# Optimization experiments

Measured on AMD Instinct MI355X. Metric: run time of the kernel, lower is better.

Reference implementation:

```python
import jax, jax.numpy as jnp
import numpy as np

VOCAB, EMB, HID = 50000, 128, 128
BATCH, SEQ = 256, 2048


def setup_inputs() -> dict:
    key = jax.random.key(0)
    k1, k2, k3, k4, k5 = jax.random.split(key, 5)
    x = jax.random.randint(k1, (BATCH, SEQ), 0, VOCAB, dtype=jnp.int32)
    emb_table = jax.random.normal(k2, (VOCAB, EMB), dtype=jnp.float32) * 0.05
    # Keras GRU (reset_after=True): kernel (EMB, 3H), recurrent_kernel (H, 3H),
    # bias (2, 3H) = [input_bias, recurrent_bias]; gate order z, r, h.
    W = jax.random.normal(k3, (EMB, 3 * HID), dtype=jnp.float32) * (1.0 / np.sqrt(EMB))
    U = jax.random.normal(k4, (HID, 3 * HID), dtype=jnp.float32) * (1.0 / np.sqrt(HID))
    b = jax.random.normal(k5, (2, 3 * HID), dtype=jnp.float32) * 0.01
    return {"x": x, "emb_table": emb_table, "W": W, "U": U, "b": b}


def _gru_scan(emb, W, U, b):
    # emb: (B, T, E). Precompute all input projections in one big GEMM.
    B, T, _ = emb.shape
    H = U.shape[0]
    xw = jnp.einsum("bte,eh->bth", emb, W) + b[0]  # (B, T, 3H)

    def step(h, xw_t):
        rh = h @ U + b[1]                      # (B, 3H) recurrent projection
        xz, xr, xh = jnp.split(xw_t, 3, axis=-1)
        uz, ur, uh = jnp.split(rh, 3, axis=-1)
        z = jax.nn.sigmoid(xz + uz)
        r = jax.nn.sigmoid(xr + ur)
        hh = jnp.tanh(xh + r * uh)             # reset_after=True candidate
        h_new = z * h + (1.0 - z) * hh
        return h_new, h_new

    h0 = jnp.zeros((B, H), dtype=emb.dtype)
    state, outs = jax.lax.scan(step, h0, jnp.swapaxes(xw, 0, 1))  # outs: (T, B, H)
    return jnp.swapaxes(outs, 0, 1), state


def reference(x, emb_table, W, U, b):
    emb = emb_table[x]                         # (B, T, E) embedding gather
    output, state = _gru_scan(emb, W, U, b)
    # V1 and V2 compute identical math -> diff is exactly zero.
    max_diff = jnp.zeros((), dtype=output.dtype)
    outputs_close = jnp.array(True)
    return output, state, outputs_close, max_diff
```

## Files before the change

### kernel.cpp

```cpp
#include <hip/hip_runtime.h>

#define B_ 256
#define T_ 2048
#define E_ 128
#define H_ 128
#define NC 384

typedef short bf16x8 __attribute__((ext_vector_type(8)));
typedef float f32x4  __attribute__((ext_vector_type(4)));

#define MF(A_, B2_, C_) __builtin_amdgcn_mfma_f32_16x16x32_bf16((A_), (B2_), (C_), 0, 0, 0)

static __device__ __forceinline__ unsigned short f2bf(float f) {
    unsigned u = __builtin_bit_cast(unsigned, f);
    return (unsigned short)((u + 0x7FFFu + ((u >> 16) & 1u)) >> 16);
}
static __device__ __forceinline__ float bf2f(unsigned short h) {
    unsigned u = (unsigned)h << 16;
    return __builtin_bit_cast(float, u);
}
static __device__ __forceinline__ float xhalf(float v, int addr) {
    return __builtin_bit_cast(float,
        __builtin_amdgcn_ds_bpermute(addr, __builtin_bit_cast(int, v)));
}
static __device__ __forceinline__ float fexp2(float x) {
    float r;
    asm("v_exp_f32 %0, %1" : "=v"(r) : "v"(x));
    return r;
}
static __device__ __forceinline__ float frcp(float x) {
    float r;
    asm("v_rcp_f32 %0, %1" : "=v"(r) : "v"(x));
    return r;
}

__global__ __launch_bounds__(512) __attribute__((amdgpu_waves_per_eu(2, 2)))
void gru_xw_mfma(
    const int*   __restrict__ x,
    const float* __restrict__ emb,
    const float* __restrict__ W,
    const float* __restrict__ bias,
    unsigned short* __restrict__ xw,
    int t0, int nsteps)
{
    const int p    = blockIdx.x;
    const int tid  = threadIdx.x;
    const int w    = tid >> 6;
    const int lane = tid & 63;
    const int rowA = lane & 15;
    const int q    = lane >> 4;
    const int mh   = w >> 2;
    const int nq   = w & 3;

    __shared__ unsigned short A_lds[2][64 * 128];

    bf16x8 Wf[6][4];
    float bf6[6]; int offn[6];
    #pragma unroll
    for (int nt = 0; nt < 6; ++nt) {
        const int col = nq * 96 + nt * 16 + rowA;
        const int g = col >> 7, cc = col & 127;
        bf6[nt]  = bias[col] + (g < 2 ? bias[NC + col] : 0.f);
        offn[nt] = (g == 2) ? (256 + cc) : ((cc << 1) + g);
        #pragma unroll
        for (int kt = 0; kt < 4; ++kt)
            #pragma unroll
            for (int e = 0; e < 8; ++e) {
                const int k = (kt << 5) + ((e >> 2) << 4) + (q << 2) + (e & 3);
                Wf[nt][kt][e] = (short)f2bf(W[(size_t)k * NC + col]);
            }
    }

    const int niter = nsteps >> 6;
    const int r_st  = tid >> 3;
    const int j_st  = tid & 7;

    #pragma unroll 1
    for (int it = 0; it < niter; ++it) {
        const int rowbase = p * nsteps + (it << 6);

        {
            const int row_local = rowbase + r_st;
            const int tloc = row_local >> 8, bb = row_local & 255;
            const int token = x[bb * T_ + t0 + tloc];
            const float* erow = emb + (size_t)token * E_;
            unsigned* dst = (unsigned*)A_lds[it & 1];
            const int mt = r_st >> 4, rA = r_st & 15;
            #pragma unroll
            for (int s = 0; s < 8; ++s) {
                const int p2 = j_st + (s << 3);
                const float2 ev = *(const float2*)(erow + (p2 << 1));
                const int kt = p2 >> 4, hi = (p2 >> 3) & 1;
                const int qq = (p2 >> 1) & 3, l0 = p2 & 1;
                const int dw = (((mt << 2) + kt) * 64 + rA + (qq << 4)) * 4
                             + (hi << 1) + l0;
                dst[dw] = (unsigned)f2bf(ev.x) | ((unsigned)f2bf(ev.y) << 16);
            }
        }
        asm volatile("s_waitcnt lgkmcnt(0)" ::: "memory");
        __builtin_amdgcn_s_barrier();
        asm volatile("" ::: "memory");

        const unsigned short* src = A_lds[it & 1];
        bf16x8 Af[2][4];
        #pragma unroll
        for (int ml = 0; ml < 2; ++ml)
            #pragma unroll
            for (int kt = 0; kt < 4; ++kt)
                Af[ml][kt] = *(const bf16x8*)(src +
                    ((((2 * mh + ml) << 2) + kt) * 64 + lane) * 8);

        f32x4 acc[2][6];
        #pragma unroll
        for (int ml = 0; ml < 2; ++ml)
            #pragma unroll
            for (int nt = 0; nt < 6; ++nt) {
                f32x4 a = {0.f, 0.f, 0.f, 0.f};
                a = MF(Af[ml][0], Wf[nt][0], a);
                a = MF(Af[ml][1], Wf[nt][1], a);
                a = MF(Af[ml][2], Wf[nt][2], a);
                a = MF(Af[ml][3], Wf[nt][3], a);
                acc[ml][nt] = a;
            }

        #pragma unroll
        for (int ml = 0; ml < 2; ++ml)
            #pragma unroll
            for (int reg = 0; reg < 4; ++reg) {
                const int m = (mh << 5) + (ml << 4) + (q << 2) + reg;
                const int row_local = rowbase + m;
                const int tloc = row_local >> 8, bb = row_local & 255;
                unsigned short* orow = xw + ((size_t)tloc * B_ + bb) * 384;
                #pragma unroll
                for (int nt = 0; nt < 6; ++nt)
                    orow[offn[nt]] = f2bf(acc[ml][nt][reg] + bf6[nt]);
            }
    }
}

__global__ __launch_bounds__(256) __attribute__((amdgpu_waves_per_eu(1, 1)))
void gru_rec_kernel(
    const unsigned short* __restrict__ xw,
    const float* __restrict__ U,
    const float* __restrict__ bias,
    float*       __restrict__ out,
    float*       __restrict__ hstate,
    int t0, int nsteps, int last)
{
    const int b   = blockIdx.x;
    const int tid = threadIdx.x;
    const int w   = tid >> 6;
    const int l   = tid & 63;
    const int col = (w << 5) + (l & 31);
    const int kh  = l >> 5;

    __shared__ __align__(16) unsigned h_pk[2][64];
    __shared__ __align__(16) unsigned short xwt[2][8][384];

    unsigned Upk[3][32];
    #pragma unroll
    for (int g = 0; g < 3; ++g) {
        #pragma unroll
        for (int j = 0; j < 32; ++j) {
            const int k = (kh << 6) + (j << 1);
            const unsigned short lo = f2bf(U[(size_t)k * NC + (g << 7) + col]);
            const unsigned short hi = f2bf(U[(size_t)(k + 1) * NC + (g << 7) + col]);
            Upk[g][j] = (unsigned)lo | ((unsigned)hi << 16);
        }
    }

    const float b1h = bias[NC + 256 + col];
    float hreg = (t0 == 0) ? 0.f : hstate[(b << 7) + col];
    if (l < 32) ((unsigned short*)h_pk[0])[col] = f2bf(hreg);

    const int srow = tid >> 5;
    const int sj   = tid & 31;
    const unsigned short* ld0 = xw + ((size_t)srow * B_ + b) * 384 + sj * 12;
    uint2 sA = *(const uint2*)(ld0);
    uint2 sB = *(const uint2*)(ld0 + 4);
    uint2 sC = *(const uint2*)(ld0 + 8);
    {
        unsigned short* dst = &xwt[0][srow][sj * 12];
        *(uint2*)dst = sA; *(uint2*)(dst + 4) = sB; *(uint2*)(dst + 8) = sC;
    }
    const int ntiles = nsteps >> 3;
    if (1 < ntiles) {
        const unsigned short* p1 = xw + ((size_t)(8 + srow) * B_ + b) * 384 + sj * 12;
        sA = *(const uint2*)(p1); sB = *(const uint2*)(p1 + 4); sC = *(const uint2*)(p1 + 8);
    }
    __syncthreads();

    float* outb = out + ((size_t)b * T_ + t0) * H_;
    const int xaddr = (l ^ 32) << 2;
    const float NL2E = -1.4426950408889634f;
    const float P2L2E = 2.8853900817779268f;

#define RSTEP(GS, XROW)                                                        \
    do {                                                                       \
        const uint4* hsrc = (const uint4*)(h_pk[(GS) & 1] + (kh << 5));        \
        const uint4 q0 = hsrc[0], q1 = hsrc[1], q2 = hsrc[2], q3 = hsrc[3];    \
        const uint4 q4 = hsrc[4], q5 = hsrc[5], q6 = hsrc[6], q7 = hsrc[7];    \
        const unsigned hd[32] = {q0.x, q0.y, q0.z, q0.w, q1.x, q1.y, q1.z, q1.w,\
                                 q2.x, q2.y, q2.z, q2.w, q3.x, q3.y, q3.z, q3.w,\
                                 q4.x, q4.y, q4.z, q4.w, q5.x, q5.y, q5.z, q5.w,\
                                 q6.x, q6.y, q6.z, q6.w, q7.x, q7.y, q7.z, q7.w};\
        const int zr = *(const int*)((XROW) + (col << 1));            \
        const unsigned short xh16 = (XROW)[256 + col];                \
        float a0 = 0.f, a1 = 0.f, a2 = 0.f;                                    \
        float c0 = 0.f, c1 = 0.f, c2 = 0.f;                                    \
        _Pragma("unroll")                                                      \
        for (int j = 0; j < 32; j += 2) {                                      \
            asm("v_dot2_f32_bf16 %0, %1, %2, %0"                               \
                : "+v"(a0) : "v"(Upk[0][j]), "v"(hd[j]));                      \
            asm("v_dot2_f32_bf16 %0, %1, %2, %0"                               \
                : "+v"(a1) : "v"(Upk[1][j]), "v"(hd[j]));                      \
            asm("v_dot2_f32_bf16 %0, %1, %2, %0"                               \
                : "+v"(a2) : "v"(Upk[2][j]), "v"(hd[j]));                      \
            asm("v_dot2_f32_bf16 %0, %1, %2, %0"                               \
                : "+v"(c0) : "v"(Upk[0][j + 1]), "v"(hd[j + 1]));              \
            asm("v_dot2_f32_bf16 %0, %1, %2, %0"                               \
                : "+v"(c1) : "v"(Upk[1][j + 1]), "v"(hd[j + 1]));              \
            asm("v_dot2_f32_bf16 %0, %1, %2, %0"                               \
                : "+v"(c2) : "v"(Upk[2][j + 1]), "v"(hd[j + 1]));              \
        }                                                                      \
        a0 += c0; a1 += c1; a2 += c2;                                          \
        a0 += xhalf(a0, xaddr);             \
        a1 += xhalf(a1, xaddr);                                                \
        a2 += xhalf(a2, xaddr);                                                \
        const float xz = bf2f((unsigned short)(zr & 0xFFFF));                  \
        const float xr = bf2f((unsigned short)((unsigned)zr >> 16));           \
        const float xh = bf2f(xh16);                                           \
        const float z = frcp(1.f + fexp2(NL2E * (xz + a0)));                   \
        const float r = frcp(1.f + fexp2(NL2E * (xr + a1)));                   \
        float aa = xh + r * (a2 + b1h);                                        \
        aa = fminf(30.f, fmaxf(-30.f, aa));                                    \
        const float e2 = fexp2(P2L2E * aa);                                    \
        const float th = 1.f - 2.f * frcp(e2 + 1.f);                           \
        hreg = z * hreg + (1.f - z) * th;                                      \
        if (l < 32) {                                                          \
            ((unsigned short*)h_pk[((GS) + 1) & 1])[col] = f2bf(hreg);         \
            outb[(size_t)(GS) * H_ + col] = hreg;         \
        }                                                                      \
        asm volatile("s_waitcnt lgkmcnt(0)" ::: "memory");                     \
        __builtin_amdgcn_s_barrier();                                          \
        asm volatile("" ::: "memory");                                         \
    } while (0)

    #pragma unroll 1
    for (int tile = 0; tile < ntiles; ++tile) {
        const int cur = tile & 1;
        if (tile + 1 < ntiles) {
            unsigned short* dst = &xwt[cur ^ 1][srow][sj * 12];
            *(uint2*)dst = sA; *(uint2*)(dst + 4) = sB; *(uint2*)(dst + 8) = sC;
            if (tile + 2 < ntiles) {
                const unsigned short* pn =
                    xw + ((size_t)((tile + 2) * 8 + srow) * B_ + b) * 384 + sj * 12;
                sA = *(const uint2*)(pn);
                sB = *(const uint2*)(pn + 4);
                sC = *(const uint2*)(pn + 8);
            }
        }
        const int gbase = tile << 3;
        #pragma unroll
        for (int s = 0; s < 8; ++s) {
            RSTEP(gbase + s, &xwt[cur][s][0]);
        }
    }
#undef RSTEP

    if (l < 32) {
        hstate[(b << 7) + col] = hreg;
        if (last) out[(size_t)B_ * T_ * H_ + (b << 7) + col] = hreg;
    }
    if (last && b == 0 && tid == 0) {
        const size_t base = (size_t)B_ * T_ * H_ + (size_t)B_ * H_;
        out[base]     = 1.0f;
        out[base + 1] = 0.0f;
    }
}

extern "C" void kernel_launch(void* const* d_in, const int* in_sizes, int n_in,
                              void* d_out, int out_size, void* d_ws, size_t ws_size,
                              hipStream_t stream)
{
    const int*   x   = (const int*)  d_in[0];
    const float* emb = (const float*)d_in[1];
    const float* W   = (const float*)d_in[2];
    const float* U   = (const float*)d_in[3];
    const float* bi  = (const float*)d_in[4];
    float* out = (float*)d_out;

    unsigned short* xwbuf = (unsigned short*)d_ws;
    const size_t perstep = (size_t)B_ * 384 * sizeof(unsigned short);
    const size_t hbytes  = (size_t)B_ * H_ * sizeof(float);

    size_t avail = (ws_size > hbytes) ? (ws_size - hbytes) : 0;
    long long chunk_ll = (long long)(avail / perstep);
    int chunk = (chunk_ll > T_) ? T_ : (int)chunk_ll;
    chunk &= ~63;
    if (chunk < 64) chunk = 64;

    float* hstate = (float*)((char*)d_ws + (size_t)chunk * perstep);

    for (int t0 = 0; t0 < T_; t0 += chunk) {
        const int n = (T_ - t0 < chunk) ? (T_ - t0) : chunk;
        const int last = (t0 + n >= T_) ? 1 : 0;
        hipLaunchKernelGGL(gru_xw_mfma, dim3(B_), dim3(512), 0, stream,
                           x, emb, W, bi, xwbuf, t0, n);
        hipLaunchKernelGGL(gru_rec_kernel, dim3(B_), dim3(256), 0, stream,
                           xwbuf, U, bi, out, hstate, t0, n, last);
    }
}
```

Before: 1.184 ms.

## Assign one thread per hidden column in recurrent GRU kernel, drop cross-lane reduce

The recurrent kernel now uses 128 threads per block, with each thread computing the full 128-long dot products for its column instead of splitting K across two half-waves. This removes the ds_bpermute reduction and halves the number of waves synchronising at each per-step barrier. Packing bf16 h pairs into LDS uses a DPP lane swap, and xw staging uses wider 16-byte loads. The trade-off is twice as many serial dot2 instructions and LDS reads per thread on the per-step critical path, plus higher register use for U.

```diff
diff --git a/kernel.cpp b/kernel.cpp
--- a/kernel.cpp
+++ b/kernel.cpp
@@ -19,9 +19,8 @@
     unsigned u = (unsigned)h << 16;
     return __builtin_bit_cast(float, u);
 }
-static __device__ __forceinline__ float xhalf(float v, int addr) {
-    return __builtin_bit_cast(float,
-        __builtin_amdgcn_ds_bpermute(addr, __builtin_bit_cast(int, v)));
+static __device__ __forceinline__ unsigned dpp_x1_u(unsigned v) {
+    return (unsigned)__builtin_amdgcn_mov_dpp((int)v, 0xB1, 0xF, 0xF, true);
 }
 static __device__ __forceinline__ float fexp2(float x) {
     float r;
@@ -138,7 +137,7 @@
     }
 }
 
-__global__ __launch_bounds__(256) __attribute__((amdgpu_waves_per_eu(1, 1)))
+__global__ __launch_bounds__(128) __attribute__((amdgpu_waves_per_eu(1, 1)))
 void gru_rec_kernel(
     const unsigned short* __restrict__ xw,
     const float* __restrict__ U,
@@ -149,20 +148,17 @@
 {
     const int b   = blockIdx.x;
     const int tid = threadIdx.x;
-    const int w   = tid >> 6;
-    const int l   = tid & 63;
-    const int col = (w << 5) + (l & 31);
-    const int kh  = l >> 5;
+    const int col = tid;
 
     __shared__ __align__(16) unsigned h_pk[2][64];
     __shared__ __align__(16) unsigned short xwt[2][8][384];
 
-    unsigned Upk[3][32];
+    unsigned Upk[3][64];
     #pragma unroll
     for (int g = 0; g < 3; ++g) {
         #pragma unroll
-        for (int j = 0; j < 32; ++j) {
-            const int k = (kh << 6) + (j << 1);
+        for (int j = 0; j < 64; ++j) {
+            const int k = j << 1;
             const unsigned short lo = f2bf(U[(size_t)k * NC + (g << 7) + col]);
             const unsigned short hi = f2bf(U[(size_t)(k + 1) * NC + (g << 7) + col]);
             Upk[g][j] = (unsigned)lo | ((unsigned)hi << 16);
@@ -171,76 +167,83 @@
 
     const float b1h = bias[NC + 256 + col];
     float hreg = (t0 == 0) ? 0.f : hstate[(b << 7) + col];
-    if (l < 32) ((unsigned short*)h_pk[0])[col] = f2bf(hreg);
-
-    const int srow = tid >> 5;
-    const int sj   = tid & 31;
-    const unsigned short* ld0 = xw + ((size_t)srow * B_ + b) * 384 + sj * 12;
-    uint2 sA = *(const uint2*)(ld0);
-    uint2 sB = *(const uint2*)(ld0 + 4);
-    uint2 sC = *(const uint2*)(ld0 + 8);
     {
-        unsigned short* dst = &xwt[0][srow][sj * 12];
-        *(uint2*)dst = sA; *(uint2*)(dst + 4) = sB; *(uint2*)(dst + 8) = sC;
+        const unsigned me = (unsigned)f2bf(hreg);
+        const unsigned pk = me | (dpp_x1_u(me) << 16);
+        if (!(col & 1)) h_pk[0][col >> 1] = pk;
+    }
+
+    const int srow = tid >> 4;
+    const int sj   = tid & 15;
+    const unsigned short* ld0 = xw + ((size_t)srow * B_ + b) * 384 + sj * 24;
+    uint4 sA = *(const uint4*)(ld0);
+    uint4 sB = *(const uint4*)(ld0 + 8);
+    uint4 sC = *(const uint4*)(ld0 + 16);
+    {
+        unsigned short* dst = &xwt[0][srow][sj * 24];
+        *(uint4*)dst = sA; *(uint4*)(dst + 8) = sB; *(uint4*)(dst + 16) = sC;
     }
     const int ntiles = nsteps >> 3;
     if (1 < ntiles) {
-        const unsigned short* p1 = xw + ((size_t)(8 + srow) * B_ + b) * 384 + sj * 12;
-        sA = *(const uint2*)(p1); sB = *(const uint2*)(p1 + 4); sC = *(const uint2*)(p1 + 8);
+        const unsigned short* p1 =
+            xw + ((size_t)(8 + srow) * B_ + b) * 384 + sj * 24;
+        sA = *(const uint4*)(p1); sB = *(const uint4*)(p1 + 8); sC = *(const uint4*)(p1 + 16);
     }
     __syncthreads();
 
     float* outb = out + ((size_t)b * T_ + t0) * H_;
-    const int xaddr = (l ^ 32) << 2;
     const float NL2E = -1.4426950408889634f;
     const float P2L2E = 2.8853900817779268f;
 
 #define RSTEP(GS, XROW)                                                        \
     do {                                                                       \
-        const uint4* hsrc = (const uint4*)(h_pk[(GS) & 1] + (kh << 5));        \
-        const uint4 q0 = hsrc[0], q1 = hsrc[1], q2 = hsrc[2], q3 = hsrc[3];    \
-        const uint4 q4 = hsrc[4], q5 = hsrc[5], q6 = hsrc[6], q7 = hsrc[7];    \
-        const unsigned hd[32] = {q0.x, q0.y, q0.z, q0.w, q1.x, q1.y, q1.z, q1.w,\
-                                 q2.x, q2.y, q2.z, q2.w, q3.x, q3.y, q3.z, q3.w,\
-                                 q4.x, q4.y, q4.z, q4.w, q5.x, q5.y, q5.z, q5.w,\
-                                 q6.x, q6.y, q6.z, q6.w, q7.x, q7.y, q7.z, q7.w};\
-        const int zr = *(const int*)((XROW) + (col << 1));            \
-        const unsigned short xh16 = (XROW)[256 + col];                \
-        float a0 = 0.f, a1 = 0.f, a2 = 0.f;                                    \
-        float c0 = 0.f, c1 = 0.f, c2 = 0.f;                                    \
+        const uint4* hsrc = (const uint4*)h_pk[(GS) & 1];                      \
+        float az0 = 0.f, ar0 = 0.f, ah0 = 0.f;                                 \
+        float az1 = 0.f, ar1 = 0.f, ah1 = 0.f;                                 \
         _Pragma("unroll")                                                      \
-        for (int j = 0; j < 32; j += 2) {                                      \
-            asm("v_dot2_f32_bf16 %0, %1, %2, %0"                               \
-                : "+v"(a0) : "v"(Upk[0][j]), "v"(hd[j]));                      \
-            asm("v_dot2_f32_bf16 %0, %1, %2, %0"                               \
-                : "+v"(a1) : "v"(Upk[1][j]), "v"(hd[j]));                      \
-            asm("v_dot2_f32_bf16 %0, %1, %2, %0"                               \
-                : "+v"(a2) : "v"(Upk[2][j]), "v"(hd[j]));                      \
-            asm("v_dot2_f32_bf16 %0, %1, %2, %0"                               \
-                : "+v"(c0) : "v"(Upk[0][j + 1]), "v"(hd[j + 1]));              \
-            asm("v_dot2_f32_bf16 %0, %1, %2, %0"                               \
-                : "+v"(c1) : "v"(Upk[1][j + 1]), "v"(hd[j + 1]));              \
-            asm("v_dot2_f32_bf16 %0, %1, %2, %0"                               \
-                : "+v"(c2) : "v"(Upk[2][j + 1]), "v"(hd[j + 1]));              \
+        for (int c4 = 0; c4 < 4; ++c4) {            \
+            const uint4 hq0 = hsrc[(c4 << 2) + 0];                             \
+            const uint4 hq1 = hsrc[(c4 << 2) + 1];                             \
+            const uint4 hq2 = hsrc[(c4 << 2) + 2];                             \
+            const uint4 hq3 = hsrc[(c4 << 2) + 3];                             \
+            const unsigned hv[16] = {hq0.x, hq0.y, hq0.z, hq0.w,               \
+                                     hq1.x, hq1.y, hq1.z, hq1.w,               \
+                                     hq2.x, hq2.y, hq2.z, hq2.w,               \
+                                     hq3.x, hq3.y, hq3.z, hq3.w};              \
+            _Pragma("unroll")                                                  \
+            for (int i = 0; i < 16; i += 2) {                                  \
+                const int j = (c4 << 4) + i;                                   \
+                asm("v_dot2_f32_bf16 %0, %1, %2, %0"                           \
+                    : "+v"(az0) : "v"(Upk[0][j]), "v"(hv[i]));                 \
+                asm("v_dot2_f32_bf16 %0, %1, %2, %0"                           \
+                    : "+v"(ar0) : "v"(Upk[1][j]), "v"(hv[i]));                 \
+                asm("v_dot2_f32_bf16 %0, %1, %2, %0"                           \
+                    : "+v"(ah0) : "v"(Upk[2][j]), "v"(hv[i]));                 \
+                asm("v_dot2_f32_bf16 %0, %1, %2, %0"                           \
+                    : "+v"(az1) : "v"(Upk[0][j + 1]), "v"(hv[i + 1]));         \
+                asm("v_dot2_f32_bf16 %0, %1, %2, %0"                           \
+                    : "+v"(ar1) : "v"(Upk[1][j + 1]), "v"(hv[i + 1]));         \
+                asm("v_dot2_f32_bf16 %0, %1, %2, %0"                           \
+                    : "+v"(ah1) : "v"(Upk[2][j + 1]), "v"(hv[i + 1]));         \
+            }                                                                  \
         }                                                                      \
-        a0 += c0; a1 += c1; a2 += c2;                                          \
-        a0 += xhalf(a0, xaddr);             \
-        a1 += xhalf(a1, xaddr);                                                \
-        a2 += xhalf(a2, xaddr);                                                \
+        const float s0 = az0 + az1, s1 = ar0 + ar1, s2 = ah0 + ah1;            \
+        const int zr = ((const int*)(XROW))[col];                              \
+        const unsigned short xh16 = (XROW)[256 + col];                         \
         const float xz = bf2f((unsigned short)(zr & 0xFFFF));                  \
         const float xr = bf2f((unsigned short)((unsigned)zr >> 16));           \
         const float xh = bf2f(xh16);                                           \
-        const float z = frcp(1.f + fexp2(NL2E * (xz + a0)));                   \
-        const float r = frcp(1.f + fexp2(NL2E * (xr + a1)));                   \
-        float aa = xh + r * (a2 + b1h);                                        \
+        const float z = frcp(1.f + fexp2(NL2E * (xz + s0)));                   \
+        const float r = frcp(1.f + fexp2(NL2E * (xr + s1)));                   \
+        float aa = xh + r * (s2 + b1h);                                        \
         aa = fminf(30.f, fmaxf(-30.f, aa));                                    \
         const float e2 = fexp2(P2L2E * aa);                                    \
         const float th = 1.f - 2.f * frcp(e2 + 1.f);                           \
         hreg = z * hreg + (1.f - z) * th;                                      \
-        if (l < 32) {                                                          \
-            ((unsigned short*)h_pk[((GS) + 1) & 1])[col] = f2bf(hreg);         \
-            outb[(size_t)(GS) * H_ + col] = hreg;         \
-        }                                                                      \
+        const unsigned me = (unsigned)f2bf(hreg);                              \
+        const unsigned pk = me | (dpp_x1_u(me) << 16);                         \
+        if (!(col & 1)) h_pk[((GS) + 1) & 1][col >> 1] = pk;                   \
+        outb[(size_t)(GS) * H_ + col] = hreg;             \
         asm volatile("s_waitcnt lgkmcnt(0)" ::: "memory");                     \
         __builtin_amdgcn_s_barrier();                                          \
         asm volatile("" ::: "memory");                                         \
@@ -250,14 +253,14 @@
     for (int tile = 0; tile < ntiles; ++tile) {
         const int cur = tile & 1;
         if (tile + 1 < ntiles) {
-            unsigned short* dst = &xwt[cur ^ 1][srow][sj * 12];
-            *(uint2*)dst = sA; *(uint2*)(dst + 4) = sB; *(uint2*)(dst + 8) = sC;
+            unsigned short* dst = &xwt[cur ^ 1][srow][sj * 24];
+            *(uint4*)dst = sA; *(uint4*)(dst + 8) = sB; *(uint4*)(dst + 16) = sC;
             if (tile + 2 < ntiles) {
                 const unsigned short* pn =
-                    xw + ((size_t)((tile + 2) * 8 + srow) * B_ + b) * 384 + sj * 12;
-                sA = *(const uint2*)(pn);
-                sB = *(const uint2*)(pn + 4);
-                sC = *(const uint2*)(pn + 8);
+                    xw + ((size_t)((tile + 2) * 8 + srow) * B_ + b) * 384 + sj * 24;
+                sA = *(const uint4*)(pn);
+                sB = *(const uint4*)(pn + 8);
+                sC = *(const uint4*)(pn + 16);
             }
         }
         const int gbase = tile << 3;
@@ -268,10 +271,8 @@
     }
 #undef RSTEP
 
-    if (l < 32) {
-        hstate[(b << 7) + col] = hreg;
-        if (last) out[(size_t)B_ * T_ * H_ + (b << 7) + col] = hreg;
-    }
+    hstate[(b << 7) + col] = hreg;
+    if (last) out[(size_t)B_ * T_ * H_ + (b << 7) + col] = hreg;
     if (last && b == 0 && tid == 0) {
         const size_t base = (size_t)B_ * T_ * H_ + (size_t)B_ * H_;
         out[base]     = 1.0f;
@@ -307,7 +308,7 @@
         const int last = (t0 + n >= T_) ? 1 : 0;
         hipLaunchKernelGGL(gru_xw_mfma, dim3(B_), dim3(512), 0, stream,
                            x, emb, W, bi, xwbuf, t0, n);
-        hipLaunchKernelGGL(gru_rec_kernel, dim3(B_), dim3(256), 0, stream,
+        hipLaunchKernelGGL(gru_rec_kernel, dim3(B_), dim3(128), 0, stream,
                            xwbuf, U, bi, out, hstate, t0, n, last);
     }
 }
```

After: 1.488 ms. +25.6%, slower.
